# Kernel tuning notes

Measured on AMD Instinct MI355X. Metric: run time of the kernel, lower is better.

The kernel has to match this reference:

```python
import jax, jax.numpy as jnp
import numpy as np
from jax import lax

DIM = 256
HEAD_DIM = 64          # v head dim and hedgehog dim
HEAD_DIM_QK = 64       # must equal HEAD_DIM for the module to run
NH = DIM // HEAD_DIM   # 4
EPS = 1e-6


def setup_inputs() -> dict:
    key = jax.random.key(0)
    ks = jax.random.split(key, 12)
    B, C, H, W, D = 1, DIM, 16, 16, 16
    x = jax.random.normal(ks[0], (B, C, H, W, D), dtype=jnp.float32)
    qk_dim = HEAD_DIM_QK * NH
    # 1x1x1 conv weights for q, k (qkv_bias=False)
    Wq = jax.random.normal(ks[1], (qk_dim, C), dtype=jnp.float32) * 0.02
    Wk = jax.random.normal(ks[2], (qk_dim, C), dtype=jnp.float32) * 0.02
    # depthwise 3x3x3 conv for v (groups=dim, bias=True)
    Wv = jax.random.normal(ks[3], (C, 1, 3, 3, 3), dtype=jnp.float32) * 0.1
    bv = jax.random.normal(ks[4], (C,), dtype=jnp.float32) * 0.02
    # HedgeHog linear layers (init is identity/zeros; use near-identity + noise)
    eye = jnp.eye(HEAD_DIM, dtype=jnp.float32)
    Wmq = eye * 0.5 + jax.random.normal(ks[5], (HEAD_DIM, HEAD_DIM), dtype=jnp.float32) * 0.02
    bmq = jnp.zeros((HEAD_DIM,), dtype=jnp.float32)
    Wmk = eye * 0.5 + jax.random.normal(ks[6], (HEAD_DIM, HEAD_DIM), dtype=jnp.float32) * 0.02
    bmk = jnp.zeros((HEAD_DIM,), dtype=jnp.float32)
    Wmv = eye * 0.5 + jax.random.normal(ks[7], (HEAD_DIM, HEAD_DIM), dtype=jnp.float32) * 0.02
    bmv = jnp.zeros((HEAD_DIM,), dtype=jnp.float32)
    return {"x": x, "Wq": Wq, "Wk": Wk, "Wv": Wv, "bv": bv,
            "Wmq": Wmq, "bmq": bmq, "Wmk": Wmk, "bmk": bmk,
            "Wmv": Wmv, "bmv": bmv}


def _hedgehog(z, W, b):
    # z: [B, nh, N, d] -> [B, 2*nh, N, d]; cat along HEAD axis (dim=1) as in torch code
    h = jnp.einsum('bhnd,ed->bhne', z, W) + b
    return jnp.concatenate([jnp.exp(h), jnp.exp(-h)], axis=1)


def reference(x, Wq, Wk, Wv, bv, Wmq, bmq, Wmk, bmk, Wmv, bmv):
    B, C, H, W_, D = x.shape
    N = H * W_ * D
    x2 = x.reshape(B, C, N)
    # 1x1x1 conv projections
    q = jnp.einsum('oc,bcn->bon', Wq, x2)  # [B, qk_dim, N]
    k = jnp.einsum('oc,bcn->bon', Wk, x2)
    # depthwise 3x3x3 conv for v
    v3 = lax.conv_general_dilated(
        x, Wv, window_strides=(1, 1, 1),
        padding=((1, 1), (1, 1), (1, 1)),
        dimension_numbers=('NCDHW', 'OIDHW', 'NCDHW'),
        feature_group_count=C) + bv[None, :, None, None, None]
    v = v3.reshape(B, C, N)
    # split heads, tokens-last -> tokens axis
    q1 = q.reshape(B, NH, HEAD_DIM_QK, N).transpose(0, 1, 3, 2)  # [B,nh,N,dqk]
    k1 = k.reshape(B, NH, HEAD_DIM_QK, N).transpose(0, 1, 3, 2)
    v1 = v.reshape(B, NH, HEAD_DIM, N).transpose(0, 1, 3, 2)     # [B,nh,N,dv]
    qf = _hedgehog(q1, Wmq, bmq)  # [B,2nh,N,dqk]
    kf = _hedgehog(k1, Wmk, bmk)
    vf = _hedgehog(v1, Wmv, bmv)  # [B,2nh,N,dv]
    # quadratic "linear" attention: row-sum normalized QK^T
    qk = jnp.einsum('bhmd,bhnd->bhmn', qf, kf)          # [B,2nh,N,N]
    attn = qk / (jnp.sum(qk, axis=-1, keepdims=True) + EPS)
    out = jnp.einsum('bhmn,bhnd->bhmd', attn, vf)        # [B,2nh,N,dv]
    out = out.transpose(0, 1, 3, 2).reshape(B, 2 * C, H, W_, D)
    return out
```

## Files before the change

### kernel.cpp

```cpp
#include <hip/hip_runtime.h>
#include <math.h>

#define EPS_F 1e-6f

#define OFF_WCQ 0
#define OFF_WCK (OFF_WCQ + 65536)
#define OFF_BV  (OFF_WCK + 65536)
#define OFF_VC  (OFF_BV + 256)
#define OFF_PS  (OFF_VC + 256*4096)
#define OFF_PSV (OFF_PS + 8*64*4096)
#define OFF_SM  (OFF_PSV + 8*64*64)
#define OFF_SV  (OFF_SM + 8*4096)
#define OFF_QF  (OFF_SV + 512)

__global__ __launch_bounds__(256) void k_combine(
    const float* __restrict__ Wq, const float* __restrict__ Wk,
    const float* __restrict__ Wmq, const float* __restrict__ Wmk,
    const float* __restrict__ Wmv, const float* __restrict__ bmv,
    const float* __restrict__ bv, float* __restrict__ ws)
{
    int row = blockIdx.x;
    int c = threadIdx.x;
    int h = row >> 6, e = row & 63;
    float aq = 0.f, ak = 0.f;
    for (int d = 0; d < 64; ++d) {
        float mq = Wmq[e*64 + d];
        float mk = Wmk[e*64 + d];
        int src = (h*64 + d)*256 + c;
        aq = fmaf(mq, Wq[src], aq);
        ak = fmaf(mk, Wk[src], ak);
    }
    ws[OFF_WCQ + row*256 + c] = aq;
    ws[OFF_WCK + row*256 + c] = ak;
    if (c == 0) {
        float av = 0.f;
        for (int d = 0; d < 64; ++d) av = fmaf(Wmv[e*64 + d], bv[h*64 + d], av);
        ws[OFF_BV + row] = av + bmv[e];
    }
}

__global__ __launch_bounds__(256) void k_dwconv(
    const float* __restrict__ x, const float* __restrict__ Wv, float* __restrict__ vc)
{
    int c = blockIdx.y;
    int n = blockIdx.x * 256 + threadIdx.x;
    int z = n >> 8, y = (n >> 4) & 15, xx = n & 15;
    const float* xc = x + c * 4096;
    const float* wc = Wv + c * 27;
    float acc = 0.f;
    #pragma unroll
    for (int kz = 0; kz < 3; ++kz) {
        int zz = z + kz - 1;
        if (zz < 0 || zz > 15) continue;
        #pragma unroll
        for (int ky = 0; ky < 3; ++ky) {
            int yy = y + ky - 1;
            if (yy < 0 || yy > 15) continue;
            #pragma unroll
            for (int kx = 0; kx < 3; ++kx) {
                int xv = xx + kx - 1;
                if (xv < 0 || xv > 15) continue;
                acc = fmaf(wc[(kz*3 + ky)*3 + kx], xc[(zz << 8) + (yy << 4) + xv], acc);
            }
        }
    }
    vc[c*4096 + n] = acc;
}

__global__ __launch_bounds__(512, 2) void k_fused(
    const float* __restrict__ X, const float* __restrict__ bmk,
    const float* __restrict__ bmq, const float* __restrict__ Wmv,
    float* __restrict__ ws)
{
    __shared__ float smem[16384];
    float (*Xs)[64]  = (float(*)[64])smem;
    float (*Wsk)[68] = (float(*)[68])(smem + 4096);
    float (*Wsq)[68] = (float(*)[68])(smem + 8448);
    float (*kfp)[64] = (float(*)[64])smem;
    float (*kfm)[64] = (float(*)[64])(smem + 4096);
    float (*vfp)[64] = (float(*)[64])(smem + 8192);
    float (*vfm)[64] = (float(*)[64])(smem + 12288);

    int t = threadIdx.x;
    int chunk = blockIdx.x;
    int hb = blockIdx.y;
    int n0 = chunk * 64;
    bool isQ = (t >= 256);
    int tl = t & 255;
    int lc = tl >> 6, ln = tl & 63;
    int e4 = (tl & 15) * 4;
    int n4 = (tl >> 4) * 4;

    float acc[4][4];
    float accV[4][4];
    #pragma unroll
    for (int i = 0; i < 4; ++i)
        #pragma unroll
        for (int j = 0; j < 4; ++j) { acc[i][j] = 0.f; accV[i][j] = 0.f; }

    const float* Wck = ws + OFF_WCK;
    const float* Wcq = ws + OFF_WCQ;
    for (int c0 = 0; c0 < 256; c0 += 64) {
        if (!isQ) {
            #pragma unroll
            for (int i = 0; i < 16; ++i)
                Xs[lc*16 + i][ln] = X[(size_t)(c0 + lc*16 + i)*4096 + n0 + ln];
        } else {
            #pragma unroll
            for (int i = 0; i < 16; ++i) {
                Wsk[ln][lc*16 + i] = Wck[(size_t)(hb*64 + lc*16 + i)*256 + c0 + ln];
                Wsq[ln][lc*16 + i] = Wcq[(size_t)(hb*64 + lc*16 + i)*256 + c0 + ln];
            }
        }
        __syncthreads();
        const float (*Wsh)[68] = isQ ? (const float (*)[68])Wsq : (const float (*)[68])Wsk;
        #pragma unroll 4
        for (int c = 0; c < 64; ++c) {
            float4 xv4 = *(const float4*)&Xs[c][n4];
            float4 wv4 = *(const float4*)&Wsh[c][e4];
            float xv[4] = {xv4.x, xv4.y, xv4.z, xv4.w};
            float wv[4] = {wv4.x, wv4.y, wv4.z, wv4.w};
            #pragma unroll
            for (int ii = 0; ii < 4; ++ii)
                #pragma unroll
                for (int jj = 0; jj < 4; ++jj)
                    acc[ii][jj] = fmaf(xv[ii], wv[jj], acc[ii][jj]);
        }
        __syncthreads();
    }

    if (!isQ) {
        const float* vcb = ws + OFF_VC + (size_t)hb*64*4096;
        #pragma unroll
        for (int i = 0; i < 16; ++i)
            Xs[lc*16 + i][ln] = vcb[(size_t)(lc*16 + i)*4096 + n0 + ln];
        #pragma unroll
        for (int i = 0; i < 16; ++i) { int idx = i*256 + tl; Wsk[idx & 63][idx >> 6] = Wmv[idx]; }
    } else {
        float* gq = ws + OFF_QF;
        #pragma unroll
        for (int jj = 0; jj < 4; ++jj) {
            float b = bmq[e4 + jj];
            float a0 = acc[0][jj] + b, a1 = acc[1][jj] + b,
                  a2 = acc[2][jj] + b, a3 = acc[3][jj] + b;
            *(float4*)&gq[(size_t)(hb*64 + e4 + jj)*4096 + n0 + n4] =
                make_float4(__expf(a0), __expf(a1), __expf(a2), __expf(a3));
            *(float4*)&gq[(size_t)((hb + 4)*64 + e4 + jj)*4096 + n0 + n4] =
                make_float4(__expf(-a0), __expf(-a1), __expf(-a2), __expf(-a3));
        }
    }
    __syncthreads();

    if (!isQ) {
        #pragma unroll 4
        for (int d = 0; d < 64; ++d) {
            float4 xv4 = *(const float4*)&Xs[d][n4];
            float4 wv4 = *(const float4*)&Wsk[d][e4];
            float xv[4] = {xv4.x, xv4.y, xv4.z, xv4.w};
            float wv[4] = {wv4.x, wv4.y, wv4.z, wv4.w};
            #pragma unroll
            for (int ii = 0; ii < 4; ++ii)
                #pragma unroll
                for (int jj = 0; jj < 4; ++jj)
                    accV[ii][jj] = fmaf(xv[ii], wv[jj], accV[ii][jj]);
        }
    }
    __syncthreads();

    if (!isQ) {
        float bk[4], bvv[4];
        #pragma unroll
        for (int j = 0; j < 4; ++j) { bk[j] = bmk[e4 + j]; bvv[j] = ws[OFF_BV + hb*64 + e4 + j]; }
        #pragma unroll
        for (int ii = 0; ii < 4; ++ii) {
            float pk[4], mk_[4], pv[4], mv[4];
            #pragma unroll
            for (int jj = 0; jj < 4; ++jj) {
                float a = acc[ii][jj] + bk[jj];
                pk[jj] = __expf(a);  mk_[jj] = __expf(-a);
                float b = accV[ii][jj] + bvv[jj];
                pv[jj] = __expf(b);  mv[jj] = __expf(-b);
            }
            *(float4*)&kfp[n4 + ii][e4] = make_float4(pk[0], pk[1], pk[2], pk[3]);
            *(float4*)&kfm[n4 + ii][e4] = make_float4(mk_[0], mk_[1], mk_[2], mk_[3]);
            *(float4*)&vfp[n4 + ii][e4] = make_float4(pv[0], pv[1], pv[2], pv[3]);
            *(float4*)&vfm[n4 + ii][e4] = make_float4(mv[0], mv[1], mv[2], mv[3]);
        }
    }
    __syncthreads();

    float aSp[4][4], aSm[4][4], svp[4], svm[4];
    #pragma unroll
    for (int i = 0; i < 4; ++i) {
        svp[i] = 0.f; svm[i] = 0.f;
        #pragma unroll
        for (int j = 0; j < 4; ++j) { aSp[i][j] = 0.f; aSm[i][j] = 0.f; }
    }
    int a4 = e4, f4 = n4;
    int nb = isQ ? 32 : 0;
    #pragma unroll 2
    for (int nn = 0; nn < 32; ++nn) {
        int n = nb + nn;
        float4 kp4 = *(const float4*)&kfp[n][a4];
        float4 km4 = *(const float4*)&kfm[n][a4];
        float4 vp4 = *(const float4*)&vfp[n][f4];
        float4 vm4 = *(const float4*)&vfm[n][f4];
        float kp[4] = {kp4.x, kp4.y, kp4.z, kp4.w};
        float km[4] = {km4.x, km4.y, km4.z, km4.w};
        float vp[4] = {vp4.x, vp4.y, vp4.z, vp4.w};
        float vm[4] = {vm4.x, vm4.y, vm4.z, vm4.w};
        #pragma unroll
        for (int ai = 0; ai < 4; ++ai) {
            svp[ai] += kp[ai];  svm[ai] += km[ai];
            #pragma unroll
            for (int fi = 0; fi < 4; ++fi) {
                aSp[ai][fi] = fmaf(kp[ai], vp[fi], aSp[ai][fi]);
                aSm[ai][fi] = fmaf(km[ai], vm[fi], aSm[ai][fi]);
            }
        }
    }
    __syncthreads();

    if (isQ) {
        #pragma unroll
        for (int i = 0; i < 4; ++i)
            #pragma unroll
            for (int j = 0; j < 4; ++j) {
                smem[(i*4 + j)*256 + tl]        = aSp[i][j];
                smem[(16 + i*4 + j)*256 + tl]   = aSm[i][j];
            }
        if (tl < 16) {
            #pragma unroll
            for (int i = 0; i < 4; ++i) {
                smem[8192 + i*16 + tl]      = svp[i];
                smem[8192 + 64 + i*16 + tl] = svm[i];
            }
        }
    }
    __syncthreads();
    if (!isQ) {
        #pragma unroll
        for (int i = 0; i < 4; ++i)
            #pragma unroll
            for (int j = 0; j < 4; ++j) {
                aSp[i][j] += smem[(i*4 + j)*256 + tl];
                aSm[i][j] += smem[(16 + i*4 + j)*256 + tl];
            }
        float* pSp = ws + OFF_PS + (size_t)(hb*64 + chunk)*4096;
        float* pSm = ws + OFF_PS + (size_t)((hb + 4)*64 + chunk)*4096;
        #pragma unroll
        for (int ai = 0; ai < 4; ++ai) {
            *(float4*)&pSp[(a4 + ai)*64 + f4] = make_float4(aSp[ai][0], aSp[ai][1], aSp[ai][2], aSp[ai][3]);
            *(float4*)&pSm[(a4 + ai)*64 + f4] = make_float4(aSm[ai][0], aSm[ai][1], aSm[ai][2], aSm[ai][3]);
        }
        if (tl < 16) {
            #pragma unroll
            for (int i = 0; i < 4; ++i) {
                svp[i] += smem[8192 + i*16 + tl];
                svm[i] += smem[8192 + 64 + i*16 + tl];
            }
            float* pvp = ws + OFF_PSV + (size_t)(hb*64 + chunk)*64;
            float* pvm = ws + OFF_PSV + (size_t)((hb + 4)*64 + chunk)*64;
            *(float4*)&pvp[a4] = make_float4(svp[0], svp[1], svp[2], svp[3]);
            *(float4*)&pvm[a4] = make_float4(svm[0], svm[1], svm[2], svm[3]);
        }
    }
}

__global__ __launch_bounds__(256) void k_reduce(float* __restrict__ ws)
{
    int idx = blockIdx.x*256 + threadIdx.x;
    if (idx < 8*4096) {
        int h = idx >> 12, r = idx & 4095;
        float s = 0.f;
        #pragma unroll 16
        for (int c = 0; c < 64; ++c) s += ws[OFF_PS + (size_t)(h*64 + c)*4096 + r];
        ws[OFF_SM + idx] = s;
    } else if (idx < 8*4096 + 512) {
        int j = idx - 8*4096;
        int h = j >> 6, e = j & 63;
        float s = 0.f;
        #pragma unroll 16
        for (int c = 0; c < 64; ++c) s += ws[OFF_PSV + (size_t)(h*64 + c)*64 + e];
        ws[OFF_SV + j] = s;
    }
}

__global__ __launch_bounds__(256, 2) void k_out(
    const float* __restrict__ ws, float* __restrict__ out)
{
    __shared__ float qs[64][64];
    __shared__ float Sms[64][64];
    __shared__ float svs[64];
    int t = threadIdx.x;
    int chunk = blockIdx.x;
    int h = blockIdx.y;
    int n0 = chunk * 64;
    int lc = t >> 6, ln = t & 63;

    const float* gq = ws + OFF_QF + (size_t)h*64*4096;
    #pragma unroll
    for (int i = 0; i < 16; ++i)
        qs[lc*16 + i][ln] = gq[(size_t)(lc*16 + i)*4096 + n0 + ln];
    const float* Smg = ws + OFF_SM + (size_t)h*4096;
    #pragma unroll
    for (int i = 0; i < 16; ++i) { int idx = i*256 + t; Sms[idx >> 6][idx & 63] = Smg[idx]; }
    if (t < 64) svs[t] = ws[OFF_SV + h*64 + t];
    __syncthreads();

    int n4 = (t & 15) * 4;
    int e4 = (t >> 4) * 4;
    float acc[4][4];
    float den[4] = {0.f, 0.f, 0.f, 0.f};
    #pragma unroll
    for (int i = 0; i < 4; ++i)
        #pragma unroll
        for (int j = 0; j < 4; ++j) acc[i][j] = 0.f;
    #pragma unroll 4
    for (int a = 0; a < 64; ++a) {
        float4 qv4 = *(const float4*)&qs[a][n4];
        float4 sm4 = *(const float4*)&Sms[a][e4];
        float qv[4] = {qv4.x, qv4.y, qv4.z, qv4.w};
        float sm[4] = {sm4.x, sm4.y, sm4.z, sm4.w};
        float sva = svs[a];
        #pragma unroll
        for (int nj = 0; nj < 4; ++nj) {
            den[nj] = fmaf(qv[nj], sva, den[nj]);
            #pragma unroll
            for (int ei = 0; ei < 4; ++ei)
                acc[ei][nj] = fmaf(sm[ei], qv[nj], acc[ei][nj]);
        }
    }
    float r[4];
    #pragma unroll
    for (int nj = 0; nj < 4; ++nj) r[nj] = 1.f / (den[nj] + EPS_F);
    #pragma unroll
    for (int ei = 0; ei < 4; ++ei)
        *(float4*)&out[(size_t)(h*64 + e4 + ei)*4096 + n0 + n4] =
            make_float4(acc[ei][0]*r[0], acc[ei][1]*r[1], acc[ei][2]*r[2], acc[ei][3]*r[3]);
}

extern "C" void kernel_launch(void* const* d_in, const int* in_sizes, int n_in,
                              void* d_out, int out_size, void* d_ws, size_t ws_size,
                              hipStream_t stream) {
    const float* x   = (const float*)d_in[0];
    const float* Wq  = (const float*)d_in[1];
    const float* Wk  = (const float*)d_in[2];
    const float* Wv  = (const float*)d_in[3];
    const float* bv  = (const float*)d_in[4];
    const float* Wmq = (const float*)d_in[5];
    const float* bmq = (const float*)d_in[6];
    const float* Wmk = (const float*)d_in[7];
    const float* bmk = (const float*)d_in[8];
    const float* Wmv = (const float*)d_in[9];
    const float* bmv = (const float*)d_in[10];
    float* out = (float*)d_out;
    float* ws  = (float*)d_ws;

    k_combine<<<256, 256, 0, stream>>>(Wq, Wk, Wmq, Wmk, Wmv, bmv, bv, ws);
    k_dwconv<<<dim3(16, 256), 256, 0, stream>>>(x, Wv, ws + OFF_VC);
    k_fused<<<dim3(64, 4), 512, 0, stream>>>(x, bmk, bmq, Wmv, ws);
    k_reduce<<<130, 256, 0, stream>>>(ws);
    k_out<<<dim3(64, 8), 256, 0, stream>>>(ws, out);
}
```

Baseline: 140.7 us.

## Use split-bf16 MFMA for Q/K projections with transposed bf16 input

Replaces the scalar FP32 FMA loop for the combined Q/K projection in the fused kernel with bf16 MFMA instructions. Precision is kept close to fp32 by splitting each value into high and low bf16 parts and issuing three MFMAs per tile. A new kernel transposes x into token-major hi/lo bf16 buffers, and the combine kernel now emits split bf16 weights. The Q feature-map stores are staged through shared memory for coalesced writes. This adds an extra launch and more workspace traffic, and the compensation drops the low×low term, giving a small accuracy loss.

```diff
diff --git a/kernel.cpp b/kernel.cpp
--- a/kernel.cpp
+++ b/kernel.cpp
@@ -3,15 +3,29 @@
 
 #define EPS_F 1e-6f
 
-#define OFF_WCQ 0
-#define OFF_WCK (OFF_WCQ + 65536)
-#define OFF_BV  (OFF_WCK + 65536)
+typedef __attribute__((ext_vector_type(8))) short bf16x8;
+typedef __attribute__((ext_vector_type(4))) float f32x4;
+
+#define OFF_BV  0
 #define OFF_VC  (OFF_BV + 256)
 #define OFF_PS  (OFF_VC + 256*4096)
 #define OFF_PSV (OFF_PS + 8*64*4096)
 #define OFF_SM  (OFF_PSV + 8*64*64)
 #define OFF_SV  (OFF_SM + 8*4096)
 #define OFF_QF  (OFF_SV + 512)
+#define OFF_WQH (OFF_QF + 512*4096)
+#define OFF_WQL (OFF_WQH + 32768)
+#define OFF_WKH (OFF_WQL + 32768)
+#define OFF_WKL (OFF_WKH + 32768)
+#define OFF_XTH (OFF_WKL + 32768)
+#define OFF_XTL (OFF_XTH + 524288)
+
+__device__ __forceinline__ void split_bf16(float v, unsigned short& h, unsigned short& l) {
+    unsigned int b = __float_as_uint(v);
+    h = (unsigned short)(b >> 16);
+    float fh = __uint_as_float(b & 0xFFFF0000u);
+    l = (unsigned short)(__float_as_uint(v - fh) >> 16);
+}
 
 __global__ __launch_bounds__(256) void k_combine(
     const float* __restrict__ Wq, const float* __restrict__ Wk,
@@ -30,13 +44,52 @@
         aq = fmaf(mq, Wq[src], aq);
         ak = fmaf(mk, Wk[src], ak);
     }
-    ws[OFF_WCQ + row*256 + c] = aq;
-    ws[OFF_WCK + row*256 + c] = ak;
+    unsigned short hh, ll;
+    unsigned short* WQH = (unsigned short*)(ws + OFF_WQH);
+    unsigned short* WQL = (unsigned short*)(ws + OFF_WQL);
+    unsigned short* WKH = (unsigned short*)(ws + OFF_WKH);
+    unsigned short* WKL = (unsigned short*)(ws + OFF_WKL);
+    split_bf16(aq, hh, ll); WQH[row*256 + c] = hh; WQL[row*256 + c] = ll;
+    split_bf16(ak, hh, ll); WKH[row*256 + c] = hh; WKL[row*256 + c] = ll;
     if (c == 0) {
         float av = 0.f;
         for (int d = 0; d < 64; ++d) av = fmaf(Wmv[e*64 + d], bv[h*64 + d], av);
         ws[OFF_BV + row] = av + bmv[e];
     }
+}
+
+__global__ __launch_bounds__(256) void k_xt(
+    const float* __restrict__ x, float* __restrict__ ws)
+{
+    __shared__ float Ts[64][65];
+    int tx = blockIdx.x;
+    int cy = blockIdx.y;
+    int t = threadIdx.x;
+    int lr = t >> 6, lc2 = t & 63;
+    #pragma unroll
+    for (int i = 0; i < 16; ++i) {
+        int row = lr*16 + i;
+        Ts[row][lc2] = x[(size_t)(cy*64 + row)*4096 + tx*64 + lc2];
+    }
+    __syncthreads();
+    int tok = t >> 2, c16 = (t & 3) * 16;
+    unsigned int hw[8], lw[8];
+    #pragma unroll
+    for (int j = 0; j < 8; ++j) {
+        float v0 = Ts[c16 + 2*j][tok], v1 = Ts[c16 + 2*j + 1][tok];
+        unsigned int b0 = __float_as_uint(v0), b1 = __float_as_uint(v1);
+        hw[j] = (b0 >> 16) | (b1 & 0xFFFF0000u);
+        float f0 = __uint_as_float(b0 & 0xFFFF0000u);
+        float f1 = __uint_as_float(b1 & 0xFFFF0000u);
+        lw[j] = (__float_as_uint(v0 - f0) >> 16) | (__float_as_uint(v1 - f1) & 0xFFFF0000u);
+    }
+    unsigned short* XH = (unsigned short*)(ws + OFF_XTH);
+    unsigned short* XL = (unsigned short*)(ws + OFF_XTL);
+    size_t base = (size_t)(tx*64 + tok)*256 + cy*64 + c16;
+    uint4 H0 = {hw[0], hw[1], hw[2], hw[3]}, H1 = {hw[4], hw[5], hw[6], hw[7]};
+    uint4 L0 = {lw[0], lw[1], lw[2], lw[3]}, L1 = {lw[4], lw[5], lw[6], lw[7]};
+    *(uint4*)(XH + base) = H0;  *(uint4*)(XH + base + 8) = H1;
+    *(uint4*)(XL + base) = L0;  *(uint4*)(XL + base + 8) = L1;
 }
 
 __global__ __launch_bounds__(256) void k_dwconv(
@@ -68,86 +121,101 @@
 }
 
 __global__ __launch_bounds__(512, 2) void k_fused(
-    const float* __restrict__ X, const float* __restrict__ bmk,
-    const float* __restrict__ bmq, const float* __restrict__ Wmv,
-    float* __restrict__ ws)
+    const float* __restrict__ bmk, const float* __restrict__ bmq,
+    const float* __restrict__ Wmv, float* __restrict__ ws)
 {
     __shared__ float smem[16384];
-    float (*Xs)[64]  = (float(*)[64])smem;
-    float (*Wsk)[68] = (float(*)[68])(smem + 4096);
-    float (*Wsq)[68] = (float(*)[68])(smem + 8448);
-    float (*kfp)[64] = (float(*)[64])smem;
-    float (*kfm)[64] = (float(*)[64])(smem + 4096);
-    float (*vfp)[64] = (float(*)[64])(smem + 8192);
-    float (*vfm)[64] = (float(*)[64])(smem + 12288);
+    unsigned short* su = (unsigned short*)smem;
 
     int t = threadIdx.x;
     int chunk = blockIdx.x;
     int hb = blockIdx.y;
     int n0 = chunk * 64;
+    int w = t >> 6, lane = t & 63;
+    int kq = w >> 2;
+    int mh = w & 1, nh = (w >> 1) & 1;
+    int l15 = lane & 15, l4 = lane >> 4;
     bool isQ = (t >= 256);
     int tl = t & 255;
     int lc = tl >> 6, ln = tl & 63;
     int e4 = (tl & 15) * 4;
     int n4 = (tl >> 4) * 4;
 
-    float acc[4][4];
+    const unsigned short* XH  = (const unsigned short*)(ws + OFF_XTH);
+    const unsigned short* XL  = (const unsigned short*)(ws + OFF_XTL);
+    const unsigned short* WKHp = (const unsigned short*)(ws + OFF_WKH);
+    const unsigned short* WKLp = (const unsigned short*)(ws + OFF_WKL);
+    const unsigned short* WQHp = (const unsigned short*)(ws + OFF_WQH);
+    const unsigned short* WQLp = (const unsigned short*)(ws + OFF_WQL);
+
+    f32x4 acc[2][2];
+    #pragma unroll
+    for (int i = 0; i < 2; ++i)
+        #pragma unroll
+        for (int j = 0; j < 2; ++j) acc[i][j] = (f32x4){0.f, 0.f, 0.f, 0.f};
     float accV[4][4];
     #pragma unroll
     for (int i = 0; i < 4; ++i)
         #pragma unroll
-        for (int j = 0; j < 4; ++j) { acc[i][j] = 0.f; accV[i][j] = 0.f; }
-
-    const float* Wck = ws + OFF_WCK;
-    const float* Wcq = ws + OFF_WCQ;
-    for (int c0 = 0; c0 < 256; c0 += 64) {
-        if (!isQ) {
-            #pragma unroll
-            for (int i = 0; i < 16; ++i)
-                Xs[lc*16 + i][ln] = X[(size_t)(c0 + lc*16 + i)*4096 + n0 + ln];
-        } else {
-            #pragma unroll
-            for (int i = 0; i < 16; ++i) {
-                Wsk[ln][lc*16 + i] = Wck[(size_t)(hb*64 + lc*16 + i)*256 + c0 + ln];
-                Wsq[ln][lc*16 + i] = Wcq[(size_t)(hb*64 + lc*16 + i)*256 + c0 + ln];
-            }
+        for (int j = 0; j < 4; ++j) accV[i][j] = 0.f;
+
+    for (int cs = 0; cs < 4; ++cs) {
+        int c0 = cs * 64;
+        {
+            int r = (t >> 3) & 63, s = t & 7;
+            unsigned short* d = su + r*64 + (((s ^ (r & 7))) << 3);
+            size_t xo = (size_t)(n0 + r)*256 + c0 + s*8;
+            size_t wo = (size_t)(hb*64 + r)*256 + c0 + s*8;
+            *(uint4*)(d)         = *(const uint4*)(XH + xo);
+            *(uint4*)(d + 4096)  = *(const uint4*)(XL + xo);
+            *(uint4*)(d + 8192)  = *(const uint4*)(WKHp + wo);
+            *(uint4*)(d + 12288) = *(const uint4*)(WKLp + wo);
+            *(uint4*)(d + 16384) = *(const uint4*)(WQHp + wo);
+            *(uint4*)(d + 20480) = *(const uint4*)(WQLp + wo);
         }
         __syncthreads();
-        const float (*Wsh)[68] = isQ ? (const float (*)[68])Wsq : (const float (*)[68])Wsk;
-        #pragma unroll 4
-        for (int c = 0; c < 64; ++c) {
-            float4 xv4 = *(const float4*)&Xs[c][n4];
-            float4 wv4 = *(const float4*)&Wsh[c][e4];
-            float xv[4] = {xv4.x, xv4.y, xv4.z, xv4.w};
-            float wv[4] = {wv4.x, wv4.y, wv4.z, wv4.w};
-            #pragma unroll
-            for (int ii = 0; ii < 4; ++ii)
+        const unsigned short* Xh = su;
+        const unsigned short* Xl = su + 4096;
+        const unsigned short* Wh = su + 8192 + kq*8192;
+        const unsigned short* Wl = Wh + 4096;
+        #pragma unroll
+        for (int ks = 0; ks < 2; ++ks) {
+            bf16x8 ah[2], al[2], bh_[2], bl_[2];
+            #pragma unroll
+            for (int mt = 0; mt < 2; ++mt) {
+                int ar = mh*32 + mt*16 + l15;
+                int off = ar*64 + (((ks*4 + l4) ^ (ar & 7)) << 3);
+                ah[mt] = *(const bf16x8*)(Xh + off);
+                al[mt] = *(const bf16x8*)(Xl + off);
+            }
+            #pragma unroll
+            for (int nt = 0; nt < 2; ++nt) {
+                int br = nh*32 + nt*16 + l15;
+                int off = br*64 + (((ks*4 + l4) ^ (br & 7)) << 3);
+                bh_[nt] = *(const bf16x8*)(Wh + off);
+                bl_[nt] = *(const bf16x8*)(Wl + off);
+            }
+            #pragma unroll
+            for (int mt = 0; mt < 2; ++mt)
                 #pragma unroll
-                for (int jj = 0; jj < 4; ++jj)
-                    acc[ii][jj] = fmaf(xv[ii], wv[jj], acc[ii][jj]);
+                for (int nt = 0; nt < 2; ++nt) {
+                    acc[mt][nt] = __builtin_amdgcn_mfma_f32_16x16x32_bf16(ah[mt], bh_[nt], acc[mt][nt], 0, 0, 0);
+                    acc[mt][nt] = __builtin_amdgcn_mfma_f32_16x16x32_bf16(al[mt], bh_[nt], acc[mt][nt], 0, 0, 0);
+                    acc[mt][nt] = __builtin_amdgcn_mfma_f32_16x16x32_bf16(ah[mt], bl_[nt], acc[mt][nt], 0, 0, 0);
+                }
         }
         __syncthreads();
     }
 
+    float (*Xs)[64]  = (float(*)[64])smem;
+    float (*Wsh)[68] = (float(*)[68])(smem + 4096);
     if (!isQ) {
         const float* vcb = ws + OFF_VC + (size_t)hb*64*4096;
         #pragma unroll
         for (int i = 0; i < 16; ++i)
             Xs[lc*16 + i][ln] = vcb[(size_t)(lc*16 + i)*4096 + n0 + ln];
         #pragma unroll
-        for (int i = 0; i < 16; ++i) { int idx = i*256 + tl; Wsk[idx & 63][idx >> 6] = Wmv[idx]; }
-    } else {
-        float* gq = ws + OFF_QF;
-        #pragma unroll
-        for (int jj = 0; jj < 4; ++jj) {
-            float b = bmq[e4 + jj];
-            float a0 = acc[0][jj] + b, a1 = acc[1][jj] + b,
-                  a2 = acc[2][jj] + b, a3 = acc[3][jj] + b;
-            *(float4*)&gq[(size_t)(hb*64 + e4 + jj)*4096 + n0 + n4] =
-                make_float4(__expf(a0), __expf(a1), __expf(a2), __expf(a3));
-            *(float4*)&gq[(size_t)((hb + 4)*64 + e4 + jj)*4096 + n0 + n4] =
-                make_float4(__expf(-a0), __expf(-a1), __expf(-a2), __expf(-a3));
-        }
+        for (int i = 0; i < 16; ++i) { int idx = i*256 + tl; Wsh[idx & 63][idx >> 6] = Wmv[idx]; }
     }
     __syncthreads();
 
@@ -155,7 +223,7 @@
         #pragma unroll 4
         for (int d = 0; d < 64; ++d) {
             float4 xv4 = *(const float4*)&Xs[d][n4];
-            float4 wv4 = *(const float4*)&Wsk[d][e4];
+            float4 wv4 = *(const float4*)&Wsh[d][e4];
             float xv[4] = {xv4.x, xv4.y, xv4.z, xv4.w};
             float wv[4] = {wv4.x, wv4.y, wv4.z, wv4.w};
             #pragma unroll
@@ -167,22 +235,37 @@
     }
     __syncthreads();
 
+    float (*kfp)[64] = (float(*)[64])smem;
+    float (*kfm)[64] = (float(*)[64])(smem + 4096);
+    float (*vfp)[64] = (float(*)[64])(smem + 8192);
+    float (*vfm)[64] = (float(*)[64])(smem + 12288);
     if (!isQ) {
-        float bk[4], bvv[4];
-        #pragma unroll
-        for (int j = 0; j < 4; ++j) { bk[j] = bmk[e4 + j]; bvv[j] = ws[OFF_BV + hb*64 + e4 + j]; }
+        float bk0 = bmk[nh*32 + l15], bk1 = bmk[nh*32 + 16 + l15];
+        #pragma unroll
+        for (int mt = 0; mt < 2; ++mt)
+            #pragma unroll
+            for (int nt = 0; nt < 2; ++nt) {
+                float bkv = nt ? bk1 : bk0;
+                int feat = nh*32 + nt*16 + l15;
+                #pragma unroll
+                for (int r = 0; r < 4; ++r) {
+                    int tok = mh*32 + mt*16 + l4*4 + r;
+                    float v = acc[mt][nt][r] + bkv;
+                    kfp[tok][feat] = __expf(v);
+                    kfm[tok][feat] = __expf(-v);
+                }
+            }
+        float bvv[4];
+        #pragma unroll
+        for (int j = 0; j < 4; ++j) bvv[j] = ws[OFF_BV + hb*64 + e4 + j];
         #pragma unroll
         for (int ii = 0; ii < 4; ++ii) {
-            float pk[4], mk_[4], pv[4], mv[4];
+            float pv[4], mv[4];
             #pragma unroll
             for (int jj = 0; jj < 4; ++jj) {
-                float a = acc[ii][jj] + bk[jj];
-                pk[jj] = __expf(a);  mk_[jj] = __expf(-a);
                 float b = accV[ii][jj] + bvv[jj];
                 pv[jj] = __expf(b);  mv[jj] = __expf(-b);
             }
-            *(float4*)&kfp[n4 + ii][e4] = make_float4(pk[0], pk[1], pk[2], pk[3]);
-            *(float4*)&kfm[n4 + ii][e4] = make_float4(mk_[0], mk_[1], mk_[2], mk_[3]);
             *(float4*)&vfp[n4 + ii][e4] = make_float4(pv[0], pv[1], pv[2], pv[3]);
             *(float4*)&vfm[n4 + ii][e4] = make_float4(mv[0], mv[1], mv[2], mv[3]);
         }
@@ -226,8 +309,8 @@
         for (int i = 0; i < 4; ++i)
             #pragma unroll
             for (int j = 0; j < 4; ++j) {
-                smem[(i*4 + j)*256 + tl]        = aSp[i][j];
-                smem[(16 + i*4 + j)*256 + tl]   = aSm[i][j];
+                smem[(i*4 + j)*256 + tl]      = aSp[i][j];
+                smem[(16 + i*4 + j)*256 + tl] = aSm[i][j];
             }
         if (tl < 16) {
             #pragma unroll
@@ -264,6 +347,39 @@
             *(float4*)&pvp[a4] = make_float4(svp[0], svp[1], svp[2], svp[3]);
             *(float4*)&pvm[a4] = make_float4(svm[0], svm[1], svm[2], svm[3]);
         }
+    }
+    __syncthreads();
+
+    float (*qTp)[68] = (float(*)[68])smem;
+    float (*qTm)[68] = (float(*)[68])(smem + 4352);
+    if (isQ) {
+        float bq0 = bmq[nh*32 + l15], bq1 = bmq[nh*32 + 16 + l15];
+        #pragma unroll
+        for (int mt = 0; mt < 2; ++mt)
+            #pragma unroll
+            for (int nt = 0; nt < 2; ++nt) {
+                float bqv = nt ? bq1 : bq0;
+                int feat = nh*32 + nt*16 + l15;
+                #pragma unroll
+                for (int r = 0; r < 4; ++r) {
+                    int tok = mh*32 + mt*16 + l4*4 + r;
+                    float v = acc[mt][nt][r] + bqv;
+                    qTp[feat][tok] = __expf(v);
+                    qTm[feat][tok] = __expf(-v);
+                }
+            }
+    }
+    __syncthreads();
+    float* gq = ws + OFF_QF;
+    #pragma unroll
+    for (int j = 0; j < 4; ++j) {
+        int un = t + 512*j;
+        int s = un >> 10;
+        int rem = un & 1023;
+        int feat = rem >> 4, t4 = (rem & 15) * 4;
+        const float* src = (s ? &qTm[feat][t4] : &qTp[feat][t4]);
+        float4 v = *(const float4*)src;
+        *(float4*)&gq[(size_t)((hb + 4*s)*64 + feat)*4096 + n0 + t4] = v;
     }
 }
 
@@ -358,8 +474,9 @@
     float* ws  = (float*)d_ws;
 
     k_combine<<<256, 256, 0, stream>>>(Wq, Wk, Wmq, Wmk, Wmv, bmv, bv, ws);
+    k_xt<<<dim3(64, 4), 256, 0, stream>>>(x, ws);
     k_dwconv<<<dim3(16, 256), 256, 0, stream>>>(x, Wv, ws + OFF_VC);
-    k_fused<<<dim3(64, 4), 512, 0, stream>>>(x, bmk, bmq, Wmv, ws);
+    k_fused<<<dim3(64, 4), 512, 0, stream>>>(bmk, bmq, Wmv, ws);
     k_reduce<<<130, 256, 0, stream>>>(ws);
     k_out<<<dim3(64, 8), 256, 0, stream>>>(ws, out);
 }
```

Result: faster. 133.2 us (-5.4%).
